# Optimization experiments

Hardware: AMD Instinct MI355X
Metric: run time of the kernel (lower is better)

The kernel has to match this reference:

```python
import jax, jax.numpy as jnp
import numpy as np

B, T, D, H = 8, 4096, 512, 512

def log_g(x):
    # log of g(x) = where(x>=0, x+0.5, sigmoid(x)) computed stably in log space
    return jnp.where(x >= 0, jnp.log(jax.nn.relu(x) + 0.5), -jax.nn.softplus(-x))

def setup_inputs() -> dict:
    key = jax.random.key(0)
    ks = jax.random.split(key, 6)
    x = jax.random.normal(ks[0], (B, T, D), dtype=jnp.float32)
    h0 = jax.random.uniform(ks[1], (B, H), dtype=jnp.float32)
    lim_z = 1.0 / np.sqrt(D)
    Wz = jax.random.uniform(ks[2], (H, D), jnp.float32, -lim_z, lim_z)
    bz = jax.random.uniform(ks[3], (H,), jnp.float32, -lim_z, lim_z)
    Wh = jax.random.uniform(ks[4], (H, D), jnp.float32, -lim_z, lim_z)
    bh = jax.random.uniform(ks[5], (H,), jnp.float32, -lim_z, lim_z)
    return {"x": x, "h0": h0, "Wz": Wz, "bz": bz, "Wh": Wh, "bh": bh}

def reference(x, h0, Wz, bz, Wh, bh):
    # gate pre-activation k: (B,T,H)
    k = jnp.einsum('btd,hd->bth', x, Wz) + bz
    log_z = -jax.nn.softplus(-k)        # log sigmoid(k)
    log_coeffs = -jax.nn.softplus(k)    # log (1 - sigmoid(k))
    log_h0 = log_g(h0)[:, None, :]      # (B,1,H)
    log_tilde_h = log_g(jnp.einsum('btd,hd->bth', x, Wh) + bh)
    # Heinsen log-space parallel scan
    log_values = jnp.concatenate([log_h0, log_z + log_tilde_h], axis=1)  # (B,T+1,H)
    a_star = jnp.pad(jnp.cumsum(log_coeffs, axis=1), ((0, 0), (1, 0), (0, 0)))  # (B,T+1,H)
    log_h = a_star + jax.lax.cumlogsumexp(log_values - a_star, axis=1)
    return jnp.exp(log_h)[:, 1:]  # (B,T,H)
```

## Files before the change

kernel.cpp:

```cpp
#include <hip/hip_runtime.h>
#include <hip/hip_fp16.h>
#include <cstdint>
#include <cstddef>

constexpr int Bb = 8, Tt = 4096, Dd = 512, Hh = 512;
constexpr int Mm = Bb * Tt;
constexpr int CHUNKS = 128;
constexpr int CLEN = Tt / CHUNKS;

typedef short short8 __attribute__((ext_vector_type(8)));
typedef float f32x4 __attribute__((ext_vector_type(4)));

#define BMT 128
#define BHT 128
#define BKT 64

__device__ inline void gload_lds16(const void* g, void* lds) {
  __builtin_amdgcn_global_load_lds(
      (const __attribute__((address_space(1))) unsigned int*)g,
      (__attribute__((address_space(3))) unsigned int*)lds,
      16, 0, 0);
}

__device__ inline unsigned short bf16_rne(float f) {
  unsigned int u = __float_as_uint(f);
  unsigned int r = (u + 0x7FFFu + ((u >> 16) & 1u)) >> 16;
  return (unsigned short)r;
}
__device__ inline uint2 pack4_bf16(const float* p) {
  uint2 hv;
  hv.x = (unsigned)bf16_rne(p[0]) | ((unsigned)bf16_rne(p[1]) << 16);
  hv.y = (unsigned)bf16_rne(p[2]) | ((unsigned)bf16_rne(p[3]) << 16);
  return hv;
}

__global__ __launch_bounds__(256) void prep_w(
    const float* __restrict__ Wz, const float* __restrict__ Wh,
    unsigned short* __restrict__ Wc) {
  int j = blockIdx.x * 256 + threadIdx.x;
  const float* src = (j < 65536) ? (Wz + (size_t)j * 4)
                                 : (Wh + (size_t)(j - 65536) * 4);
  float4 w = *(const float4*)src;
  *(uint2*)(Wc + (size_t)j * 4) = pack4_bf16((const float*)&w);
}

__device__ inline void gates_c(float kv, float pv, float& a, float& v) {
  a = 1.f / (1.f + __expf(kv));
  float z = 1.f - a;
  float g = (pv >= 0.f) ? (pv + 0.5f) : 1.f / (1.f + __expf(-pv));
  v = z * g;
}

__global__ __launch_bounds__(256, 2) void gemm_fused(
    const float* __restrict__ x, const unsigned short* __restrict__ Wc,
    const float* __restrict__ bz, const float* __restrict__ bh,
    unsigned int* __restrict__ av,
    float* __restrict__ aggA, float* __restrict__ aggH) {
  __shared__ __align__(16) char smem[49152];
  unsigned short* Abf = (unsigned short*)smem;
  unsigned short* Bzf = (unsigned short*)(smem + 16384);
  unsigned short* Bhf = (unsigned short*)(smem + 32768);
  float* AsL = (float*)smem;
  float* HsL = (float*)(smem + 16384);

  const int tid = threadIdx.x;
  const int lane = tid & 63, wid = tid >> 6;
  int swz = (blockIdx.x & 7) * 128 + (blockIdx.x >> 3);
  const int bm = swz >> 2, hn = swz & 3;
  const int row0 = bm * BMT, h0 = hn * BHT;

  const int wr = (wid >> 1) * 64, hc = (wid & 1) * 64;
  const int fr = lane & 15, kg = lane >> 4;

  const int r8 = lane >> 3;
  const int c8 = ((lane & 7) ^ r8) * 8;
  const int fr7 = lane & 7;
  const int sk0 = (kg ^ fr7) * 8;
  const int sk1 = ((kg + 4) ^ fr7) * 8;

  f32x4 ak[4][4], ap[4][4];
#pragma unroll
  for (int i = 0; i < 4; ++i)
#pragma unroll
    for (int j = 0; j < 4; ++j) { ak[i][j] = (f32x4)0.f; ap[i][j] = (f32x4)0.f; }

  for (int k0 = 0; k0 < Dd; k0 += BKT) {
    float4 avx[8];
#pragma unroll
    for (int i = 0; i < 8; ++i) {
      int f = i * 256 + tid;
      avx[i] = *(const float4*)(x + (size_t)(row0 + (f >> 4)) * Dd + k0 + (f & 15) * 4);
    }
    __syncthreads();
#pragma unroll
    for (int i = 0; i < 4; ++i) {
      int rw = wid * 32 + i * 8;
      gload_lds16(Wc + (size_t)(h0 + rw + r8) * Dd + k0 + c8, &Bzf[rw * BKT]);
      gload_lds16(Wc + (size_t)(512 + h0 + rw + r8) * Dd + k0 + c8, &Bhf[rw * BKT]);
    }
#pragma unroll
    for (int i = 0; i < 8; ++i) {
      int f = i * 256 + tid;
      int r = f >> 4;
      uint2 hv = pack4_bf16((const float*)&avx[i]);
      int soff = ((((f & 15) >> 1) ^ (r & 7)) * 8) + (f & 1) * 4;
      *(uint2*)&Abf[r * BKT + soff] = hv;
    }
    __syncthreads();

#pragma unroll
    for (int ks = 0; ks < 2; ++ks) {
      const int sk = ks ? sk1 : sk0;
      short8 fa[4], fz[4], fh[4];
#pragma unroll
      for (int mi = 0; mi < 4; ++mi)
        fa[mi] = *(const short8*)&Abf[(wr + mi * 16 + fr) * BKT + sk];
#pragma unroll
      for (int ni = 0; ni < 4; ++ni) {
        fz[ni] = *(const short8*)&Bzf[(hc + ni * 16 + fr) * BKT + sk];
        fh[ni] = *(const short8*)&Bhf[(hc + ni * 16 + fr) * BKT + sk];
      }
#pragma unroll
      for (int mi = 0; mi < 4; ++mi)
#pragma unroll
        for (int ni = 0; ni < 4; ++ni) {
          ak[mi][ni] = __builtin_amdgcn_mfma_f32_16x16x32_bf16(fa[mi], fz[ni], ak[mi][ni], 0, 0, 0);
          ap[mi][ni] = __builtin_amdgcn_mfma_f32_16x16x32_bf16(fa[mi], fh[ni], ap[mi][ni], 0, 0, 0);
        }
    }
  }

  __syncthreads();

#pragma unroll
  for (int ni = 0; ni < 4; ++ni) {
    int colG = h0 + hc + ni * 16 + fr;
    float bzv = bz[colG];
    float bhv = bh[colG];
    int cl = hc + ni * 16 + fr;
#pragma unroll
    for (int mi = 0; mi < 4; ++mi) {
      float A4 = 1.f, H4 = 0.f;
#pragma unroll
      for (int j = 0; j < 4; ++j) {
        float a, v;
        gates_c(ak[mi][ni][j] + bzv, ap[mi][ni][j] + bhv, a, v);
        int row = row0 + wr + mi * 16 + kg * 4 + j;
        unsigned int u = (unsigned int)__half_as_ushort(__float2half_rn(a)) |
                         ((unsigned int)__half_as_ushort(__float2half_rn(v)) << 16);
        av[(size_t)row * Hh + colG] = u;
        H4 = fmaf(a, H4, v);
        A4 *= a;
      }
      int srow = (wr >> 2) + mi * 4 + kg;
      AsL[srow * BHT + cl] = A4;
      HsL[srow * BHT + cl] = H4;
    }
  }
  __syncthreads();

  const int b = row0 >> 12;
  const int cbase = (row0 & 4095) >> 5;
#pragma unroll
  for (int p0 = 0; p0 < 2; ++p0) {
    int p = p0 * 256 + tid;
    int chunk = p >> 7, cl = p & 127;
    float A = 1.f, H = 0.f;
#pragma unroll
    for (int s = 0; s < 8; ++s) {
      int srow = chunk * 8 + s;
      float As = AsL[srow * BHT + cl];
      float Hs = HsL[srow * BHT + cl];
      H = fmaf(As, H, Hs);
      A *= As;
    }
    size_t idx = ((size_t)b * CHUNKS + cbase + chunk) * Hh + h0 + cl;
    aggA[idx] = A;
    aggH[idx] = H;
  }
}

__global__ __launch_bounds__(256) void scan_carry_ks(
    const float* __restrict__ aggA, const float* __restrict__ aggH,
    const float* __restrict__ h0, float* __restrict__ carry) {
  __shared__ float As[256], Hs[256];
  const int tid = threadIdx.x;
  const int c = tid & 127;
  const int gch = blockIdx.x * 2 + (tid >> 7);
  const int b = gch >> 9, h = gch & 511;
  size_t base = (size_t)b * CHUNKS * Hh + h;
  float A = aggA[base + (size_t)c * Hh];
  float H = aggH[base + (size_t)c * Hh];
  As[tid] = A; Hs[tid] = H;
  __syncthreads();
#pragma unroll
  for (int s = 1; s < 128; s <<= 1) {
    float Al = 1.f, Hl = 0.f;
    const bool act = (c >= s);
    if (act) { Al = As[tid - s]; Hl = Hs[tid - s]; }
    __syncthreads();
    if (act) {
      H = fmaf(A, Hl, H);
      A = A * Al;
      As[tid] = A; Hs[tid] = H;
    }
    __syncthreads();
  }
  float hv = h0[(size_t)b * Hh + h];
  float g0 = (hv >= 0.f) ? (hv + 0.5f) : 1.f / (1.f + __expf(-hv));
  float cr;
  if (c == 0) cr = g0;
  else cr = fmaf(As[tid - 1], g0, Hs[tid - 1]);
  carry[base + (size_t)c * Hh] = cr;
}

__global__ __launch_bounds__(512) void scan_apply_av(
    const unsigned int* __restrict__ av, const float* __restrict__ carry,
    float* __restrict__ out) {
  const int h = threadIdx.x;
  const int bc = blockIdx.x;
  const int b = bc >> 7, c = bc & 127;
  float hp = carry[(size_t)bc * Hh + h];
  size_t base = ((size_t)b * Tt + (size_t)c * CLEN) * Hh + h;
#pragma unroll
  for (int i = 0; i < CLEN; ++i) {
    size_t idx = base + (size_t)i * Hh;
    unsigned int u = av[idx];
    float a = __half2float(__ushort_as_half((unsigned short)(u & 0xFFFFu)));
    float v = __half2float(__ushort_as_half((unsigned short)(u >> 16)));
    hp = fmaf(a, hp, v);
    out[idx] = hp;
  }
}

extern "C" void kernel_launch(void* const* d_in, const int* in_sizes, int n_in,
                              void* d_out, int out_size, void* d_ws, size_t ws_size,
                              hipStream_t stream) {
  const float* x  = (const float*)d_in[0];
  const float* h0 = (const float*)d_in[1];
  const float* Wz = (const float*)d_in[2];
  const float* bz = (const float*)d_in[3];
  const float* Wh = (const float*)d_in[4];
  const float* bh = (const float*)d_in[5];
  float* out = (float*)d_out;

  char* w = (char*)d_ws;
  unsigned int* avb    = (unsigned int*)w;
  unsigned short* Wc   = (unsigned short*)(w + 67108864);
  float* aggA          = (float*)(w + 68157440);
  float* aggH          = (float*)(w + 70254592);
  float* carry         = (float*)(w + 72351744);

  const int grid = (Mm / BMT) * (Hh / BHT);
  prep_w<<<512, 256, 0, stream>>>(Wz, Wh, Wc);
  gemm_fused<<<grid, 256, 0, stream>>>(x, Wc, bz, bh, avb, aggA, aggH);
  scan_carry_ks<<<(Bb * Hh) / 2, 256, 0, stream>>>(aggA, aggH, h0, carry);
  scan_apply_av<<<Bb * CHUNKS, 512, 0, stream>>>(avb, carry, out);
}
```

Baseline: 100.3 us.

## Prefetch next x tile into registers during MFMA and swap bf16 conversion to intrinsic

The x tile for the next K step is now loaded into registers right after the current tile is written to LDS, so the global load overlaps the MFMA compute. The barrier is replaced by a hand-written s_waitcnt vmcnt(8) plus s_barrier, which waits only for the older global-to-LDS weight loads and not the new prefetch. The manual bf16 rounding is also swapped for the __float2bfloat16 intrinsic, which may map to a hardware convert. The risks are correctness if the vmcnt ordering assumption is wrong, and higher register pressure at two waves per SIMD.

```diff
diff --git a/kernel.cpp b/kernel.cpp
--- a/kernel.cpp
+++ b/kernel.cpp
@@ -1,5 +1,6 @@
 #include <hip/hip_runtime.h>
 #include <hip/hip_fp16.h>
+#include <hip/hip_bf16.h>
 #include <cstdint>
 #include <cstddef>
 
@@ -22,15 +23,16 @@
       16, 0, 0);
 }
 
-__device__ inline unsigned short bf16_rne(float f) {
-  unsigned int u = __float_as_uint(f);
-  unsigned int r = (u + 0x7FFFu + ((u >> 16) & 1u)) >> 16;
-  return (unsigned short)r;
-}
-__device__ inline uint2 pack4_bf16(const float* p) {
+__device__ inline unsigned short bf16c(float f) {
+  __hip_bfloat16 h = __float2bfloat16(f);
+  union { __hip_bfloat16 h; unsigned short u; } cv;
+  cv.h = h;
+  return cv.u;
+}
+__device__ inline uint2 pack4_cvt(const float* p) {
   uint2 hv;
-  hv.x = (unsigned)bf16_rne(p[0]) | ((unsigned)bf16_rne(p[1]) << 16);
-  hv.y = (unsigned)bf16_rne(p[2]) | ((unsigned)bf16_rne(p[3]) << 16);
+  hv.x = (unsigned)bf16c(p[0]) | ((unsigned)bf16c(p[1]) << 16);
+  hv.y = (unsigned)bf16c(p[2]) | ((unsigned)bf16c(p[3]) << 16);
   return hv;
 }
 
@@ -41,7 +43,7 @@
   const float* src = (j < 65536) ? (Wz + (size_t)j * 4)
                                  : (Wh + (size_t)(j - 65536) * 4);
   float4 w = *(const float4*)src;
-  *(uint2*)(Wc + (size_t)j * 4) = pack4_bf16((const float*)&w);
+  *(uint2*)(Wc + (size_t)j * 4) = pack4_cvt((const float*)&w);
 }
 
 __device__ inline void gates_c(float kv, float pv, float& a, float& v) {
@@ -84,13 +86,14 @@
 #pragma unroll
     for (int j = 0; j < 4; ++j) { ak[i][j] = (f32x4)0.f; ap[i][j] = (f32x4)0.f; }
 
+  float4 avx[8];
+#pragma unroll
+  for (int i = 0; i < 8; ++i) {
+    int f = i * 256 + tid;
+    avx[i] = *(const float4*)(x + (size_t)(row0 + (f >> 4)) * Dd + (f & 15) * 4);
+  }
+
   for (int k0 = 0; k0 < Dd; k0 += BKT) {
-    float4 avx[8];
-#pragma unroll
-    for (int i = 0; i < 8; ++i) {
-      int f = i * 256 + tid;
-      avx[i] = *(const float4*)(x + (size_t)(row0 + (f >> 4)) * Dd + k0 + (f & 15) * 4);
-    }
     __syncthreads();
 #pragma unroll
     for (int i = 0; i < 4; ++i) {
@@ -102,11 +105,22 @@
     for (int i = 0; i < 8; ++i) {
       int f = i * 256 + tid;
       int r = f >> 4;
-      uint2 hv = pack4_bf16((const float*)&avx[i]);
+      uint2 hv = pack4_cvt((const float*)&avx[i]);
       int soff = ((((f & 15) >> 1) ^ (r & 7)) * 8) + (f & 1) * 4;
       *(uint2*)&Abf[r * BKT + soff] = hv;
     }
-    __syncthreads();
+    asm volatile("" ::: "memory");
+    if (k0 + BKT < Dd) {
+#pragma unroll
+      for (int i = 0; i < 8; ++i) {
+        int f = i * 256 + tid;
+        avx[i] = *(const float4*)(x + (size_t)(row0 + (f >> 4)) * Dd + (k0 + BKT) + (f & 15) * 4);
+      }
+      asm volatile("s_waitcnt vmcnt(8) lgkmcnt(0)" ::: "memory");
+    } else {
+      asm volatile("s_waitcnt vmcnt(0) lgkmcnt(0)" ::: "memory");
+    }
+    asm volatile("s_barrier" ::: "memory");
 
 #pragma unroll
     for (int ks = 0; ks < 2; ++ks) {
```

Measured after the change: 101.8 us. Within noise of the previous version (+1.5%).
